# Kernel tuning notes

Hardware: AMD Instinct MI355X
Metric: run time of the kernel (lower is better)

Reference implementation:

```python
import jax, jax.numpy as jnp
import numpy as np

N_NODES = 50000
N_EDGES = 800000
IN_C, HID_C, OUT_C = 128, 128, 64


def setup_inputs() -> dict:
    key = jax.random.key(0)
    k_x, k_e, k_w1, k_w2 = jax.random.split(key, 4)
    x = jax.random.normal(k_x, (N_NODES, IN_C), dtype=jnp.float32)
    edge_index = jax.random.randint(k_e, (2, N_EDGES), 0, N_NODES, dtype=jnp.int64)
    # Glorot-style scaled weights (as in PyG GCNConv linear layers)
    W1 = jax.random.normal(k_w1, (IN_C, HID_C), dtype=jnp.float32) * (1.0 / np.sqrt(IN_C))
    b1 = jnp.zeros((HID_C,), dtype=jnp.float32)
    W2 = jax.random.normal(k_w2, (HID_C, OUT_C), dtype=jnp.float32) * (1.0 / np.sqrt(HID_C))
    b2 = jnp.zeros((OUT_C,), dtype=jnp.float32)
    return {"x": x, "edge_index": edge_index, "W1": W1, "b1": b1, "W2": W2, "b2": b2}


def _gcn_norm(edge_index, num_nodes):
    """Add self-loops and compute symmetric D^{-1/2} A D^{-1/2} edge coefficients."""
    loop = jnp.arange(num_nodes, dtype=edge_index.dtype)
    src = jnp.concatenate([edge_index[0], loop])  # [E + N]
    dst = jnp.concatenate([edge_index[1], loop])  # [E + N]
    w = jnp.ones(src.shape[0], dtype=jnp.float32)  # edge_weight=None -> ones
    deg = jax.ops.segment_sum(w, dst, num_segments=num_nodes)  # includes self-loop
    dinv = jnp.where(deg > 0, jax.lax.rsqrt(deg), 0.0)
    norm = dinv[src] * w * dinv[dst]  # [E + N]
    return src, dst, norm


def _gcn_conv(h, W, b, src, dst, norm, num_nodes):
    h = h @ W                               # [N, out] dense transform
    msg = h[src] * norm[:, None]            # [E+N, out] gather + scale
    agg = jax.ops.segment_sum(msg, dst, num_segments=num_nodes)  # scatter-add
    return agg + b


def reference(x, edge_index, W1, b1, W2, b2):
    n = x.shape[0]
    src, dst, norm = _gcn_norm(edge_index, n)
    h = _gcn_conv(x, W1, b1, src, dst, norm, n)
    h = jax.nn.relu(h)
    # dropout p=0.5 is identity in eval mode (training=False)
    return _gcn_conv(h, W2, b2, src, dst, norm, n)
```

## Files before the change

### kernel.cpp

```cpp
#include <hip/hip_runtime.h>

#define C_IN  128
#define C_HID 128
#define C_OUT 64
#define TILE  4096
#define BCAP  6144

typedef __attribute__((ext_vector_type(8))) short short8;
typedef __attribute__((ext_vector_type(4))) float f32x4;

__device__ __forceinline__ unsigned f2bf(float f) {
    unsigned u = __float_as_uint(f);
    return (u + 0x7FFF + ((u >> 16) & 1)) >> 16;
}
__device__ __forceinline__ float bflo(unsigned t) { return __uint_as_float(t << 16); }
__device__ __forceinline__ float bfhi(unsigned t) { return __uint_as_float(t & 0xFFFF0000u); }

__device__ __forceinline__ int block_exscan(int v, int* s) {
    const int tid = threadIdx.x;
    s[tid] = v;
    __syncthreads();
    #pragma unroll
    for (int off = 1; off < 256; off <<= 1) {
        int t = (tid >= off) ? s[tid - off] : 0;
        __syncthreads();
        s[tid] += t;
        __syncthreads();
    }
    return s[tid] - v;
}

__device__ __forceinline__ int block_exscan512(int v, int* s) {
    const int tid = threadIdx.x;
    s[tid] = v;
    __syncthreads();
    #pragma unroll
    for (int off = 1; off < 512; off <<= 1) {
        int t = (tid >= off) ? s[tid - off] : 0;
        __syncthreads();
        s[tid] += t;
        __syncthreads();
    }
    return s[tid] - v;
}


__global__ __launch_bounds__(256) void k_histo(const int* __restrict__ ei, int* __restrict__ histT,
                                               int E, int NT, int NB) {
    __shared__ int h[256];
    const int t = blockIdx.x;
    const int tid = threadIdx.x;
    h[tid] = 0;
    __syncthreads();
    const int end = min((t + 1) * TILE, E);
    for (int i = t * TILE + tid; i < end; i += 256)
        atomicAdd(&h[ei[E + i] >> 8], 1);
    __syncthreads();
    if (tid < NB) histT[tid * NT + t] = h[tid];
}


__global__ __launch_bounds__(256) void k_tilescan(const int* __restrict__ histT,
                                                  int* __restrict__ tilePrefix,
                                                  int* __restrict__ BT, int NT, int NB) {
    __shared__ int s[256];
    const int b = blockIdx.x;
    const int tid = threadIdx.x;
    int v = (tid < NT) ? histT[b * NT + tid] : 0;
    int ex = block_exscan(v, s);
    if (tid < NT) tilePrefix[b * NT + tid] = ex;
    if (tid == 255) BT[b] = s[255];
}


__global__ __launch_bounds__(512) void k_reorder(const int* __restrict__ ei,
                                                 const int* __restrict__ tilePrefix,
                                                 const int* __restrict__ BT,
                                                 unsigned* __restrict__ tmp,
                                                 int E, int NT, int NB) {
    __shared__ int s[512];
    __shared__ int cur[256];
    const int t = blockIdx.x;
    const int tid = threadIdx.x;
    int v = (tid < NB) ? BT[tid] : 0;
    int base = block_exscan512(v, s);
    if (tid < NB) cur[tid] = base + tilePrefix[tid * NT + t];
    __syncthreads();
    const int end = min((t + 1) * TILE, E);
    for (int i = t * TILE + tid; i < end; i += 512) {
        int d = ei[E + i];
        int sv = ei[i];
        int p = atomicAdd(&cur[d >> 8], 1);
        tmp[p] = ((unsigned)sv << 8) | (unsigned)(d & 255);
    }
}


__global__ __launch_bounds__(512) void k_bucket(const unsigned* __restrict__ tmp,
                                                const int* __restrict__ BT,
                                                int* __restrict__ row_ptr,
                                                float* __restrict__ dinv,
                                                int* __restrict__ csr_src,
                                                int E, int NB, int n) {
    __shared__ int sA[512], ssc[512];
    __shared__ int c[256], lcur[256];
    __shared__ unsigned ebuf[BCAP];
    __shared__ int obuf[BCAP];
    const int b = blockIdx.x;
    const int tid = threadIdx.x;

    int v = (tid < NB) ? BT[tid] : 0;
    (void)block_exscan512(v, sA);
    const int vb = BT[b];
    const int rbeg = sA[b] - vb;
    const bool fits = (vb <= BCAP);

    if (tid < 256) c[tid] = 0;
    __syncthreads();
    if (fits) {
        for (int i = tid; i < vb; i += 512) {
            unsigned w = tmp[rbeg + i];
            ebuf[i] = w;
            atomicAdd(&c[w & 255], 1);
        }
    } else {
        for (int i = tid; i < vb; i += 512)
            atomicAdd(&c[tmp[rbeg + i] & 255], 1);
    }
    __syncthreads();

    int cv = (tid < 256) ? c[tid] : 0;
    int ex = block_exscan512(cv, ssc);

    if (tid < 256) {
        const int d = b * 256 + tid;
        if (d < n) {
            row_ptr[d] = rbeg + ex;
            dinv[d] = rsqrtf((float)(c[tid] + 1));
            if (d == n - 1) row_ptr[n] = E;
        }
        lcur[tid] = ex;
    }
    __syncthreads();

    if (fits) {
        for (int i = tid; i < vb; i += 512) {
            unsigned w = ebuf[i];
            int p = atomicAdd(&lcur[w & 255], 1);
            obuf[p] = (int)(w >> 8);
        }
        __syncthreads();
        for (int i = tid; i < vb; i += 512)
            csr_src[rbeg + i] = obuf[i];
    } else {
        for (int i = tid; i < vb; i += 512) {
            unsigned w = tmp[rbeg + i];
            int p = atomicAdd(&lcur[w & 255], 1);
            csr_src[rbeg + p] = (int)(w >> 8);
        }
    }
}


template<int N, bool F32IN>
__global__ __launch_bounds__(256) void k_gemm_mfma(const void* __restrict__ Xraw,
                                                   const float* __restrict__ W,
                                                   const float* __restrict__ dinv,
                                                   unsigned short* __restrict__ H, int M) {
    constexpr int K = 128;
    constexpr int LDT = K + 8;
    __shared__ unsigned short sWt[N * LDT];

    const int tid = threadIdx.x;
    constexpr int NLOG = (N == 128) ? 7 : 6;
    for (int idx = tid; idx < K * N; idx += 256) {
        int k = idx >> NLOG, c = idx & (N - 1);
        sWt[c * LDT + k] = (unsigned short)f2bf(W[idx]);
    }
    __syncthreads();

    const int wave = __builtin_amdgcn_readfirstlane(tid >> 6);
    const int lane = tid & 63;
    const int m0 = blockIdx.x * 64 + wave * 16;
    if (m0 >= M) return;

    const int arow = lane & 15;
    const int koff = (lane >> 4) * 8;

    short8 a[4];
    if (F32IN) {
        const float* apf = (const float*)Xraw + (size_t)(m0 + arow) * K + koff;
        #pragma unroll
        for (int q = 0; q < 4; ++q) {
            float4 v0 = *(const float4*)(apf + q * 32);
            float4 v1 = *(const float4*)(apf + q * 32 + 4);
            short8 t;
            t[0] = (short)f2bf(v0.x); t[1] = (short)f2bf(v0.y);
            t[2] = (short)f2bf(v0.z); t[3] = (short)f2bf(v0.w);
            t[4] = (short)f2bf(v1.x); t[5] = (short)f2bf(v1.y);
            t[6] = (short)f2bf(v1.z); t[7] = (short)f2bf(v1.w);
            a[q] = t;
        }
    } else {
        const unsigned short* ap = (const unsigned short*)Xraw + (size_t)(m0 + arow) * K + koff;
        #pragma unroll
        for (int q = 0; q < 4; ++q) a[q] = *(const short8*)(ap + q * 32);
    }

    const int row0 = m0 + (lane >> 4) * 4;
    const float4 dv = *(const float4*)(dinv + row0);

    #pragma unroll
    for (int ct = 0; ct < N / 16; ++ct) {
        const int bcol = ct * 16 + (lane & 15);
        const unsigned short* bp = &sWt[bcol * LDT + koff];
        f32x4 acc = {0.f, 0.f, 0.f, 0.f};
        #pragma unroll
        for (int q = 0; q < 4; ++q) {
            short8 bq = *(const short8*)(bp + q * 32);
            acc = __builtin_amdgcn_mfma_f32_16x16x32_bf16(a[q], bq, acc, 0, 0, 0);
        }
        const int col = ct * 16 + (lane & 15);
        #pragma unroll
        for (int r = 0; r < 4; ++r) {
            float dr = (r == 0) ? dv.x : (r == 1) ? dv.y : (r == 2) ? dv.z : dv.w;
            H[(size_t)(row0 + r) * N + col] = (unsigned short)f2bf(acc[r] * dr);
        }
    }
}


template<int C, bool RELU, bool OUTBF>
__global__ __launch_bounds__(256) void k_agg(const void* __restrict__ hraw,
                                             const int* __restrict__ row_ptr,
                                             const int* __restrict__ csr_src,
                                             const float* __restrict__ dinv,
                                             const float* __restrict__ bias,
                                             void* __restrict__ agg, int n) {
    constexpr int U = 16;
    constexpr int VPC = C / 64;
    const int lane = threadIdx.x & 63;
    const int wv = __builtin_amdgcn_readfirstlane(threadIdx.x >> 6);
    const int v = blockIdx.x * 4 + wv;
    if (v >= n) return;

    const unsigned*       hu = (const unsigned*)hraw;
    const unsigned short* hs = (const unsigned short*)hraw;

    const int e0 = row_ptr[v], e1 = row_ptr[v + 1];
    const float dd = dinv[v];

    float acc[VPC];
    if (VPC == 2) {
        unsigned t = hu[(size_t)v * 64 + lane];
        acc[0] = bflo(t);
        acc[1] = bfhi(t);
    } else {
        acc[0] = bflo(hs[(size_t)v * 64 + lane]);
    }

    int j0 = e0;
    for (; j0 + U <= e1; j0 += U) {
        int ss[U];
        #pragma unroll
        for (int u = 0; u < U; ++u) ss[u] = csr_src[j0 + u];
        float hv[U][VPC];
        #pragma unroll
        for (int u = 0; u < U; ++u) {
            if (VPC == 2) {
                unsigned t = hu[(size_t)ss[u] * 64 + lane];
                hv[u][0] = bflo(t);
                hv[u][1] = bfhi(t);
            } else {
                hv[u][0] = bflo(hs[(size_t)ss[u] * 64 + lane]);
            }
        }
        #pragma unroll
        for (int u = 0; u < U; ++u) {
            acc[0] += hv[u][0];
            if (VPC == 2) acc[1] += hv[u][1];
        }
    }
    if (j0 < e1) {
        int ss[U];
        #pragma unroll
        for (int u = 0; u < U; ++u) {
            int sraw = csr_src[j0 + u];
            ss[u] = (j0 + u < e1) ? sraw : v;
        }
        float hv[U][VPC];
        #pragma unroll
        for (int u = 0; u < U; ++u) {
            if (VPC == 2) {
                unsigned t = hu[(size_t)ss[u] * 64 + lane];
                hv[u][0] = bflo(t);
                hv[u][1] = bfhi(t);
            } else {
                hv[u][0] = bflo(hs[(size_t)ss[u] * 64 + lane]);
            }
        }
        #pragma unroll
        for (int u = 0; u < U; ++u) {
            float m = (j0 + u < e1) ? 1.f : 0.f;
            acc[0] = fmaf(m, hv[u][0], acc[0]);
            if (VPC == 2) acc[1] = fmaf(m, hv[u][1], acc[1]);
        }
    }

    if (VPC == 2) {
        float2 bv = ((const float2*)bias)[lane];
        float ox = acc[0] * dd + bv.x;
        float oy = acc[1] * dd + bv.y;
        if (RELU) { ox = fmaxf(ox, 0.f); oy = fmaxf(oy, 0.f); }
        if (OUTBF) {
            ((unsigned*)agg)[(size_t)v * 64 + lane] = (f2bf(oy) << 16) | f2bf(ox);
        } else {
            ((float2*)agg)[(size_t)v * 64 + lane] = make_float2(ox, oy);
        }
    } else {
        float o = acc[0] * dd + bias[lane];
        if (RELU) o = fmaxf(o, 0.f);
        if (OUTBF) ((unsigned short*)agg)[(size_t)v * 64 + lane] = (unsigned short)f2bf(o);
        else       ((float*)agg)[(size_t)v * 64 + lane] = o;
    }
}


extern "C" void kernel_launch(void* const* d_in, const int* in_sizes, int n_in,
                              void* d_out, int out_size, void* d_ws, size_t ws_size,
                              hipStream_t stream) {
    const float* x  = (const float*)d_in[0];
    const int*   ei = (const int*)d_in[1];
    const float* W1 = (const float*)d_in[2];
    const float* b1 = (const float*)d_in[3];
    const float* W2 = (const float*)d_in[4];
    const float* b2 = (const float*)d_in[5];
    float* out = (float*)d_out;

    const int N = in_sizes[0] / C_IN;
    const int E = in_sizes[1] / 2;
    const int NT = (E + TILE - 1) / TILE;
    const int NB = (N + 255) >> 8;
    const int M2 = NB * NT;

    char* base = (char*)d_ws;
    size_t off = 0;
    auto alloc = [&](size_t bytes) {
        char* q = base + off;
        off = (off + bytes + 15) & ~(size_t)15;
        return q;
    };
    int*   histT      = (int*)  alloc((size_t)M2 * 4);
    int*   tilePrefix = (int*)  alloc((size_t)M2 * 4);
    int*   BT         = (int*)  alloc(256 * 4);
    unsigned* tmp     = (unsigned*)alloc((size_t)E * 4);
    int*   row_ptr    = (int*)  alloc((size_t)(N + 1) * 4);
    float* dinv       = (float*)alloc((size_t)N * 4);
    int*   csr_src    = (int*)  alloc((size_t)E * 4);
    unsigned short* h    = (unsigned short*)alloc((size_t)N * C_HID * 2);
    unsigned short* agg1 = (unsigned short*)alloc((size_t)N * C_HID * 2);
    unsigned short* h2   = h;

    dim3 blk(256);

    k_histo   <<<NT, blk, 0, stream>>>(ei, histT, E, NT, NB);
    k_tilescan<<<NB, blk, 0, stream>>>(histT, tilePrefix, BT, NT, NB);
    k_reorder <<<NT, dim3(512), 0, stream>>>(ei, tilePrefix, BT, tmp, E, NT, NB);
    k_bucket  <<<NB, dim3(512), 0, stream>>>(tmp, BT, row_ptr, dinv, csr_src, E, NB, N);

    const int gblocks = (N + 63) / 64;
    const int ablocks = (N + 3) / 4;

    k_gemm_mfma<C_HID, true><<<gblocks, blk, 0, stream>>>(x, W1, dinv, h, N);
    k_agg<C_HID, true, true><<<ablocks, blk, 0, stream>>>(h, row_ptr, csr_src, dinv, b1, agg1, N);

    k_gemm_mfma<C_OUT, false><<<gblocks, blk, 0, stream>>>(agg1, W2, dinv, h2, N);
    k_agg<C_OUT, false, false><<<ablocks, blk, 0, stream>>>(h2, row_ptr, csr_src, dinv, b2, out, N);
}
```

Measured before the change: 110.6 us.

## Split layer-1 aggregation into four channel slices with edge-parallel lane groups

Replaces the first-layer aggregation with a kernel that partitions the 128 bf16 channels into four 32-channel slices, each handled by a separate block. Within a wave, four 16-lane groups process different edges at once, and their partial sums are combined with cross-lane shuffles. The aim is more edges in flight per wave and a smaller per-block working set for the random gathers. In exchange, row_ptr, csr_src and dinv are read four times per node, there are four times as many blocks, and each gather is only 64 bytes.

```diff
diff --git a/kernel.cpp b/kernel.cpp
--- a/kernel.cpp
+++ b/kernel.cpp
@@ -226,6 +226,69 @@
             float dr = (r == 0) ? dv.x : (r == 1) ? dv.y : (r == 2) ? dv.z : dv.w;
             H[(size_t)(row0 + r) * N + col] = (unsigned short)f2bf(acc[r] * dr);
         }
+    }
+}
+
+
+__global__ __launch_bounds__(256) void k_agg128s(const unsigned* __restrict__ hu,
+                                                 const int* __restrict__ row_ptr,
+                                                 const int* __restrict__ csr_src,
+                                                 const float* __restrict__ dinv,
+                                                 const float* __restrict__ bias,
+                                                 unsigned* __restrict__ agg, int n) {
+    const int lane = threadIdx.x & 63;
+    const int wv = __builtin_amdgcn_readfirstlane(threadIdx.x >> 6);
+    const int slice = blockIdx.x & 3;
+    const int v = (blockIdx.x >> 2) * 4 + wv;
+    if (v >= n) return;
+
+    const int grp = lane >> 4;
+    const int cl  = lane & 15;
+    const unsigned* hsl = hu + slice * 16;
+
+    const int e0 = row_ptr[v], e1 = row_ptr[v + 1];
+    const float dd = dinv[v];
+
+    float a0 = 0.f, a1 = 0.f;
+    if (grp == 0) {
+        unsigned t = hsl[(size_t)v * 64 + cl];
+        a0 = bflo(t); a1 = bfhi(t);
+    }
+
+    int j0 = e0;
+    for (; j0 + 16 <= e1; j0 += 16) {
+        int s0 = csr_src[j0 + grp];
+        int s1 = csr_src[j0 + 4 + grp];
+        int s2 = csr_src[j0 + 8 + grp];
+        int s3 = csr_src[j0 + 12 + grp];
+        unsigned t0 = hsl[(size_t)s0 * 64 + cl];
+        unsigned t1 = hsl[(size_t)s1 * 64 + cl];
+        unsigned t2 = hsl[(size_t)s2 * 64 + cl];
+        unsigned t3 = hsl[(size_t)s3 * 64 + cl];
+        a0 += bflo(t0); a1 += bfhi(t0);
+        a0 += bflo(t1); a1 += bfhi(t1);
+        a0 += bflo(t2); a1 += bfhi(t2);
+        a0 += bflo(t3); a1 += bfhi(t3);
+    }
+    for (; j0 < e1; j0 += 4) {
+        int idx = j0 + grp;
+        bool ok = (idx < e1);
+        int s = ok ? csr_src[idx] : v;
+        unsigned t = hsl[(size_t)s * 64 + cl];
+        float m = ok ? 1.f : 0.f;
+        a0 = fmaf(m, bflo(t), a0);
+        a1 = fmaf(m, bfhi(t), a1);
+    }
+
+    a0 += __shfl_xor(a0, 16); a1 += __shfl_xor(a1, 16);
+    a0 += __shfl_xor(a0, 32); a1 += __shfl_xor(a1, 32);
+
+    if (grp == 0) {
+        float2 bv = ((const float2*)bias)[slice * 16 + cl];
+        float ox = a0 * dd + bv.x;
+        float oy = a1 * dd + bv.y;
+        ox = fmaxf(ox, 0.f); oy = fmaxf(oy, 0.f);
+        agg[(size_t)v * 64 + slice * 16 + cl] = (f2bf(oy) << 16) | f2bf(ox);
     }
 }
 
@@ -370,9 +433,11 @@
 
     const int gblocks = (N + 63) / 64;
     const int ablocks = (N + 3) / 4;
+    const int asblocks = ((N + 3) / 4) * 4;
 
     k_gemm_mfma<C_HID, true><<<gblocks, blk, 0, stream>>>(x, W1, dinv, h, N);
-    k_agg<C_HID, true, true><<<ablocks, blk, 0, stream>>>(h, row_ptr, csr_src, dinv, b1, agg1, N);
+    k_agg128s<<<asblocks, blk, 0, stream>>>((const unsigned*)h, row_ptr, csr_src, dinv, b1,
+                                            (unsigned*)agg1, N);
 
     k_gemm_mfma<C_OUT, false><<<gblocks, blk, 0, stream>>>(agg1, W2, dinv, h2, N);
     k_agg<C_OUT, false, false><<<ablocks, blk, 0, stream>>>(h2, row_ptr, csr_src, dinv, b2, out, N);
```

Measured after the change: 163.7 us. 48.0% more time.
